# Performance work log

Measured on AMD Instinct MI355X. Metric: run time of the kernel, lower is better.

Reference implementation:

```python
import jax, jax.numpy as jnp
import numpy as np

B, H, W, C = 2, 128, 128, 96
L = H * W
NUM_HEADS = 6
D_STATE = 16
DT_RANK = 6  # ceil(96/16)
D_CONV = 4
MLP_HIDDEN = 4 * C


def _layernorm(x, g, b, eps=1e-5):
    m = x.mean(-1, keepdims=True)
    v = x.var(-1, keepdims=True)
    return (x - m) * jax.lax.rsqrt(v + eps) * g + b


def _dwconv2d(x, w, b):
    # x: [B,C,H,W], w: [C,1,3,3] depthwise, padding=1 (torch 'same' for k=3)
    y = jax.lax.conv_general_dilated(x, w, (1, 1), [(1, 1), (1, 1)],
                                     dimension_numbers=('NCHW', 'OIHW', 'NCHW'),
                                     feature_group_count=x.shape[1])
    return y + b[None, :, None, None]


def _dwconv1d(x, w):
    # x: [B,C,L], w: [C,1,4]; torch padding='same' for even k=4 pads (1,2); bias is None (conv_bias//2 == 0)
    return jax.lax.conv_general_dilated(x, w, (1,), [(1, 2)],
                                        dimension_numbers=('NCH', 'OIH', 'NCH'),
                                        feature_group_count=x.shape[1])


def _rope(x):
    # x: [b, H, W, c]; 2D axial rotary embedding, k_max = c//4 per axis
    b, h, w, c = x.shape
    k_max = c // 4
    theta = 1.0 / (10000.0 ** (jnp.arange(k_max, dtype=jnp.float32) / k_max))
    ang_h = jnp.broadcast_to(jnp.arange(h, dtype=jnp.float32)[:, None, None] * theta, (h, w, k_max))
    ang_w = jnp.broadcast_to(jnp.arange(w, dtype=jnp.float32)[None, :, None] * theta, (h, w, k_max))
    angles = jnp.concatenate([ang_h, ang_w], -1)  # [h,w,c//2]
    cos, sin = jnp.cos(angles), jnp.sin(angles)
    xr, xi = x[..., 0::2], x[..., 1::2]  # consecutive pairs -> complex
    out_r = xr * cos - xi * sin
    out_i = xr * sin + xi * cos
    return jnp.stack([out_r, out_i], -1).reshape(x.shape)


def _linear_attention(x, qk_w, qk_b, lepe_w, lepe_b):
    # x: [b, n, c]
    b, n, c = x.shape
    hd = c // NUM_HEADS
    qk = x @ qk_w + qk_b  # [b,n,2c]
    q = jax.nn.elu(qk[..., :c]) + 1.0
    k = jax.nn.elu(qk[..., c:]) + 1.0
    v = x
    q_r = _rope(q.reshape(b, H, W, c)).reshape(b, n, NUM_HEADS, hd).transpose(0, 2, 1, 3)
    k_r = _rope(k.reshape(b, H, W, c)).reshape(b, n, NUM_HEADS, hd).transpose(0, 2, 1, 3)
    qh = q.reshape(b, n, NUM_HEADS, hd).transpose(0, 2, 1, 3)
    kh = k.reshape(b, n, NUM_HEADS, hd).transpose(0, 2, 1, 3)
    vh = v.reshape(b, n, NUM_HEADS, hd).transpose(0, 2, 1, 3)
    kmean = kh.mean(axis=2, keepdims=True)  # [b,h,1,hd]
    zden = 1.0 / (jnp.einsum('bhnd,bhmd->bhnm', qh, kmean) + 1e-6)  # [b,h,n,1]
    scale = n ** (-0.5)
    kv = jnp.einsum('bhnd,bhne->bhde', k_r * scale, vh * scale)  # [b,h,hd,hd]
    out = jnp.einsum('bhnd,bhde->bhne', q_r, kv) * zden
    out = out.transpose(0, 2, 1, 3).reshape(b, n, c)
    v2d = v.reshape(b, H, W, c).transpose(0, 3, 1, 2)
    lepe = _dwconv2d(v2d, lepe_w, lepe_b).transpose(0, 2, 3, 1).reshape(b, n, c)
    return out + lepe


def _selective_scan(u, delta, A, Bm, Cm, Dv):
    # u, delta: [b,d,l]; A: [d,n]; Bm, Cm: [b,n,l]; Dv: [d]
    dA = jnp.exp(jnp.einsum('bdl,dn->lbdn', delta, A))
    dBu = jnp.einsum('bdl,bnl,bdl->lbdn', delta, Bm, u)
    Ct = jnp.moveaxis(Cm, -1, 0)  # [l,b,n]

    def step(hcar, inp):
        dA_t, dBu_t, C_t = inp
        hcar = dA_t * hcar + dBu_t  # [b,d,n]
        y_t = jnp.einsum('bdn,bn->bd', hcar, C_t)
        return hcar, y_t

    h0 = jnp.zeros(dA.shape[1:], dtype=u.dtype)
    _, ys = jax.lax.scan(step, h0, (dA, dBu, Ct))  # ys: [l,b,d]
    y = jnp.moveaxis(ys, 0, -1)  # [b,d,l]
    return y + Dv[None, :, None] * u


def setup_inputs() -> dict:
    key = jax.random.key(0)
    ks = iter(jax.random.split(key, 40))

    def rn(shape, s=0.02):
        return jax.random.normal(next(ks), shape, jnp.float32) * s

    dt = jnp.exp(jax.random.uniform(next(ks), (C,), jnp.float32)
                 * (np.log(0.1) - np.log(0.001)) + np.log(0.001))
    dt_proj_b = dt + jnp.log(-jnp.expm1(-dt))
    return {
        'hidden_states': jax.random.normal(next(ks), (B, L, C), jnp.float32),
        'norm_in_g': jnp.ones((C,), jnp.float32),
        'norm_in_b': jnp.zeros((C,), jnp.float32),
        'in_proj_w': rn((C, 3 * C)),
        'dw_w': rn((C, 1, 3, 3)),
        'dw_b': rn((C,)),
        'qk_w': rn((C, 2 * C)),
        'qk_b': rn((2 * C,)),
        'lepe_w': rn((C, 1, 3, 3)),
        'lepe_b': rn((C,)),
        'conv_x_w': rn((C, 1, D_CONV)),
        'conv_z_w': rn((C, 1, D_CONV)),
        'x_proj_w': rn((C, DT_RANK + 2 * D_STATE)),
        'dt_proj_w': rn((DT_RANK, C), DT_RANK ** -0.5),
        'dt_proj_b': dt_proj_b,
        'A_log': jnp.log(jnp.broadcast_to(jnp.arange(1, D_STATE + 1, dtype=jnp.float32), (C, D_STATE)) + 0.0),
        'D': jnp.ones((C,), jnp.float32),
        'out_proj_w': rn((2 * C, C)),
        'proj_out_w': rn((C, C)),
        'proj_out_b': rn((C,)),
        'out_w': rn((2 * C, C)),
        'out_b': rn((C,)),
        'norm_mlp_g': jnp.ones((C,), jnp.float32),
        'norm_mlp_b': jnp.zeros((C,), jnp.float32),
        'fc1_w': rn((C, MLP_HIDDEN)),
        'fc1_b': rn((MLP_HIDDEN,)),
        'fc2_w': rn((MLP_HIDDEN, C)),
        'fc2_b': rn((C,)),
    }


def reference(hidden_states, norm_in_g, norm_in_b, in_proj_w, dw_w, dw_b, qk_w, qk_b,
              lepe_w, lepe_b, conv_x_w, conv_z_w, x_proj_w, dt_proj_w, dt_proj_b,
              A_log, D, out_proj_w, proj_out_w, proj_out_b, out_w, out_b,
              norm_mlp_g, norm_mlp_b, fc1_w, fc1_b, fc2_w, fc2_b):
    b, l, c = hidden_states.shape
    shortcut = hidden_states
    hs = _layernorm(hidden_states, norm_in_g, norm_in_b)
    xzw = jnp.transpose(hs @ in_proj_w, (0, 2, 1))  # [b,3c,l]
    x, z, w_ = jnp.split(xzw, 3, axis=1)  # each [b,c,l]
    # linear-attention branch
    lin_x = jax.nn.silu(_dwconv2d(w_.reshape(b, c, H, W), dw_w, dw_b))
    lin_x = jnp.transpose(lin_x, (0, 2, 3, 1)).reshape(b, l, c)
    lin_x = _linear_attention(lin_x, qk_w, qk_b, lepe_w, lepe_b)
    # selective-scan branch
    A = -jnp.exp(A_log)
    x = jax.nn.silu(_dwconv1d(x, conv_x_w))
    z = jax.nn.silu(_dwconv1d(z, conv_z_w))
    x_dbl = jnp.einsum('bdl,de->ble', x, x_proj_w)
    dt = x_dbl[..., :DT_RANK]
    Bm = jnp.transpose(x_dbl[..., DT_RANK:DT_RANK + D_STATE], (0, 2, 1))
    Cm = jnp.transpose(x_dbl[..., DT_RANK + D_STATE:], (0, 2, 1))
    delta = jax.nn.softplus(jnp.einsum('blr,rd->bdl', dt, dt_proj_w) + dt_proj_b[None, :, None])
    y = _selective_scan(x, delta, A, Bm, Cm, D)
    y = jnp.concatenate([y, z], axis=1)  # [b,2c,l]
    out1 = jnp.transpose(y, (0, 2, 1)) @ out_proj_w  # [b,l,c]
    z_t = jnp.transpose(z, (0, 2, 1))
    out2 = (lin_x * z_t) @ proj_out_w + proj_out_b
    out = jnp.concatenate([out1, out2], -1) @ out_w + out_b
    out = shortcut + out
    h2 = _layernorm(out, norm_mlp_g, norm_mlp_b)
    h2 = jax.nn.gelu(h2 @ fc1_w + fc1_b, approximate=False)
    return out + (h2 @ fc2_w + fc2_b)
```

## Files before the change

kernel.cpp:

```cpp
#include <hip/hip_runtime.h>
#include <hip/hip_bf16.h>
#include <math.h>

#define B_ 2
#define H_ 128
#define W_ 128
#define C_ 96
#define L_ (H_*W_)
#define BL_ (B_*L_)
#define NH_ 6
#define NPROJ_ 38
#define MLPH_ 384
#define NCH_ 512
#define CHL_ (L_/NCH_)
#define NG_ 32

typedef __attribute__((ext_vector_type(8))) short bf16x8;
typedef __attribute__((ext_vector_type(4))) float f32x4;

#define MFMA16(a,b,c) __builtin_amdgcn_mfma_f32_16x16x32_bf16(a,b,c,0,0,0)

#define WOFF1 0
#define WOFF2 54
#define WOFF3 90
#define WOFF4 126
#define WOFF5 144
#define WOFF6 180
#define WOFF7 252
#define WOFF8 324
#define WFRAGS 333

__device__ __forceinline__ float siluf(float x){ return x / (1.f + __expf(-x)); }
__device__ __forceinline__ unsigned short f2bf(float x){
    __hip_bfloat16 h = __float2bfloat16(x);
    return *reinterpret_cast<unsigned short*>(&h);
}
__device__ __forceinline__ unsigned pack2(float a, float b){
    return (unsigned)f2bf(a) | ((unsigned)f2bf(b) << 16);
}
__device__ __forceinline__ float bf2f(unsigned short u){
    return __uint_as_float((unsigned)u << 16);
}
__device__ __forceinline__ float gelu_fast(float x){
    float u_ = 0.7978845608f*x*(1.f + 0.044715f*x*x);
    float au = fabsf(u_);
    float e = __expf(-2.f*au);
    float th = (1.f - e)/(1.f + e);
    th = copysignf(th, u_);
    return 0.5f*x*(1.f + th);
}

__global__ __launch_bounds__(64) void k_setup(const float* __restrict__ w1,
    const float* __restrict__ w2, const float* __restrict__ w3,
    const float* __restrict__ w4, const float* __restrict__ w5,
    const float* __restrict__ w6, const float* __restrict__ w7,
    const float* __restrict__ dww, const float* __restrict__ lw,
    const float* __restrict__ xpw, const float* __restrict__ cxw,
    const float* __restrict__ czw,
    unsigned short* __restrict__ dst, float2* __restrict__ ctab,
    float* __restrict__ wt9, float* __restrict__ lw9, float* __restrict__ kvacc,
    float* __restrict__ wxT, float* __restrict__ wzT)
{
    int m = blockIdx.y;
    int l = threadIdx.x;
    if (m < 7){
        const float* srcs[7] = {w1,w2,w3,w4,w5,w6,w7};
        const int Ks[7]   = {96,96,192,96,192,96,384};
        const int Ns[7]   = {288,192,96,96,96,384,96};
        const int offs[7] = {WOFF1,WOFF2,WOFF3,WOFF4,WOFF5,WOFF6,WOFF7};
        int f = blockIdx.x;
        int nnt = Ns[m] >> 4, nkf = Ks[m] >> 5;
        if (f >= nnt*nkf) return;
        int kf = f / nnt, nt = f - kf*nnt;
        const float* s = srcs[m];
        unsigned short* d = dst + ((size_t)(offs[m] + f)*64 + l)*8;
        int krow = kf*32 + (l>>4)*8;
        int col  = nt*16 + (l&15);
        #pragma unroll
        for (int j=0;j<8;j++) d[j] = f2bf(s[(size_t)(krow+j)*Ns[m] + col]);
    } else {
        int x = blockIdx.x;
        if (x == 0){
            for (int i=l; i<128*24; i+=64){
                int pos = i/24, p = i%24;
                float th = powf(10000.f, -(float)p/24.f);
                float sn, cs; sincosf((float)pos*th, &sn, &cs);
                ctab[i] = make_float2(cs, sn);
            }
        } else if (x == 1){
            for (int i=l; i<3264; i+=64) kvacc[i] = 0.f;
        } else if (x == 2){
            for (int i=l; i<864; i+=64){
                int c = i/9, tap = i%9;
                wt9[tap*96 + c] = dww[i];
                lw9[tap*96 + c] = lw[i];
            }
        } else if (x == 3){
            for (int f=0; f<9; f++){
                int kf=f/3, nt=f%3;
                unsigned short* d = dst + ((size_t)(WOFF8 + f)*64 + l)*8;
                int krow = kf*32 + (l>>4)*8;
                int col  = nt*16 + (l&15);
                #pragma unroll
                for (int j=0;j<8;j++){
                    float v = (col < NPROJ_) ? xpw[(size_t)(krow+j)*NPROJ_ + col] : 0.f;
                    d[j] = f2bf(v);
                }
            }
        } else if (x == 4){
            for (int i=l; i<384; i+=64){
                int j = i/96, c = i%96;
                wxT[i] = cxw[c*4 + j];
                wzT[i] = czw[c*4 + j];
            }
        }
    }
}

__global__ __launch_bounds__(256) void k_ln_inproj_m(const float* __restrict__ hs,
    const float* __restrict__ gg, const float* __restrict__ bb,
    const unsigned short* __restrict__ wbf,
    float* __restrict__ xx, float* __restrict__ zz, float* __restrict__ ww)
{
    __shared__ unsigned short A[64*128];
    int t = threadIdx.x;
    size_t row0 = (size_t)blockIdx.x * 64;
    {
        int r = t >> 2, q = t & 3;
        const float* src = hs + (row0 + r)*C_ + q*24;
        float v[24];
        float s=0.f, s2=0.f;
        #pragma unroll
        for (int i=0;i<24;i++){ float x=src[i]; v[i]=x; s+=x; s2+=x*x; }
        s += __shfl_xor(s,1); s2 += __shfl_xor(s2,1);
        s += __shfl_xor(s,2); s2 += __shfl_xor(s2,2);
        float mn = s*(1.f/C_);
        float rs = rsqrtf(s2*(1.f/C_) - mn*mn + 1e-5f);
        int base = r*128, sw = (r&7)<<3;
        #pragma unroll
        for (int i=0;i<24;i+=2){
            int c = q*24 + i;
            float a0 = (v[i]  -mn)*rs*gg[c]   + bb[c];
            float a1 = (v[i+1]-mn)*rs*gg[c+1] + bb[c+1];
            *(unsigned*)&A[base + (c ^ sw)] = pack2(a0,a1);
        }
    }
    __syncthreads();
    int w = t>>6, l = t&63, lr = l&15, lh = l>>4;
    int arow = w*16 + lr;
    int abase = arow*128, asw = (arow&7)<<3;
    bf16x8 af[3];
    #pragma unroll
    for (int kf=0;kf<3;kf++)
        af[kf] = *(const bf16x8*)&A[abase + ((kf*32 + lh*8) ^ asw)];
    #pragma unroll 2
    for (int nt=0; nt<18; nt++){
        f32x4 acc = {0.f,0.f,0.f,0.f};
        #pragma unroll
        for (int kf=0;kf<3;kf++){
            bf16x8 bf_ = *(const bf16x8*)(wbf + ((size_t)((WOFF1 + kf*18 + nt)*64 + l))*8);
            acc = MFMA16(af[kf], bf_, acc);
        }
        float* base_;
        if (nt < 6) base_ = xx; else if (nt < 12) base_ = zz; else base_ = ww;
        int col = (nt%6)*16 + lr;
        float* dst = base_ + (row0 + w*16 + lh*4)*C_ + col;
        #pragma unroll
        for (int j=0;j<4;j++) dst[(size_t)j*C_] = acc[j];
    }
}

__global__ __launch_bounds__(256) void k_dwconv2d(const float* __restrict__ wwb,
    const float* __restrict__ wt9, const float* __restrict__ dwb,
    float* __restrict__ out)
{
    int gid = blockIdx.x*256 + threadIdx.x;
    int row = gid/24, c4 = gid%24; int c = c4*4;
    int b = row >> 14;
    int ll = row & (L_-1);
    int h = ll >> 7, wq = ll & 127;
    float4 acc = {0.f,0.f,0.f,0.f};
    #pragma unroll
    for (int kh=0; kh<3; kh++){
        int hh = h + kh - 1;
        if ((unsigned)hh < 128u){
            int base_row = (b<<14) + (hh<<7);
            #pragma unroll
            for (int kw=0; kw<3; kw++){
                int wp = wq + kw - 1;
                if ((unsigned)wp < 128u){
                    float4 v = *(const float4*)&wwb[(size_t)(base_row + wp)*C_ + c];
                    float4 wt = *(const float4*)&wt9[(kh*3+kw)*96 + c];
                    acc.x += v.x*wt.x; acc.y += v.y*wt.y;
                    acc.z += v.z*wt.z; acc.w += v.w*wt.w;
                }
            }
        }
    }
    float4 bv = *(const float4*)&dwb[c];
    float4 o;
    o.x = siluf(acc.x+bv.x); o.y = siluf(acc.y+bv.y);
    o.z = siluf(acc.z+bv.z); o.w = siluf(acc.w+bv.w);
    *(float4*)&out[(size_t)row*C_ + c] = o;
}

__global__ __launch_bounds__(256) void k_conv1d_xdbl(const float* __restrict__ xxb,
    const float* __restrict__ zzb, const float* __restrict__ wxT,
    const float* __restrict__ wzT, const unsigned short* __restrict__ wbf,
    const float* __restrict__ dtw, const float* __restrict__ dtb,
    float* __restrict__ xs, float* __restrict__ zs,
    float* __restrict__ delta, float* __restrict__ BC)
{
    __shared__ unsigned short A[64*128];
    __shared__ float XD[64][8];
    __shared__ float dtws[6][96];
    int t = threadIdx.x;
    size_t row0 = (size_t)blockIdx.x * 64;
    int b = (int)(row0 >> 14);
    int l0 = (int)(row0 & 16383);
    for (int i=t; i<576; i+=256) dtws[i/96][i%96] = dtw[i];
    for (int p=t; p<64*24; p+=256){
        int r = p/24, cq = p - r*24, c = cq*4;
        int l = l0 + r;
        float ax0=0.f,ax1=0.f,ax2=0.f,ax3=0.f;
        float az0=0.f,az1=0.f,az2=0.f,az3=0.f;
        #pragma unroll
        for (int j=0;j<4;j++){
            int lq = l - 1 + j;
            if ((unsigned)lq < (unsigned)L_){
                size_t off = ((size_t)(b<<14) + lq)*C_ + c;
                float4 xv = *(const float4*)&xxb[off];
                float4 zv = *(const float4*)&zzb[off];
                float4 wx4 = *(const float4*)&wxT[j*96 + c];
                float4 wz4 = *(const float4*)&wzT[j*96 + c];
                ax0 += xv.x*wx4.x; ax1 += xv.y*wx4.y; ax2 += xv.z*wx4.z; ax3 += xv.w*wx4.w;
                az0 += zv.x*wz4.x; az1 += zv.y*wz4.y; az2 += zv.z*wz4.z; az3 += zv.w*wz4.w;
            }
        }
        ax0=siluf(ax0); ax1=siluf(ax1); ax2=siluf(ax2); ax3=siluf(ax3);
        az0=siluf(az0); az1=siluf(az1); az2=siluf(az2); az3=siluf(az3);
        float4 xo={ax0,ax1,ax2,ax3}, zo={az0,az1,az2,az3};
        *(float4*)&xs[(row0+r)*C_ + c] = xo;
        *(float4*)&zs[(row0+r)*C_ + c] = zo;
        int sw = (r&7)<<3;
        uint2 pk = { pack2(ax0,ax1), pack2(ax2,ax3) };
        *(uint2*)&A[r*128 + (c ^ sw)] = pk;
    }
    __syncthreads();
    int w=t>>6, l=t&63, lr=l&15, lh=l>>4;
    int arow = w*16+lr, asw=(arow&7)<<3;
    bf16x8 af[3];
    #pragma unroll
    for (int kf=0;kf<3;kf++)
        af[kf] = *(const bf16x8*)&A[arow*128 + ((kf*32 + lh*8) ^ asw)];
    #pragma unroll
    for (int nt=0; nt<3; nt++){
        f32x4 acc={0.f,0.f,0.f,0.f};
        #pragma unroll
        for (int kf=0;kf<3;kf++){
            bf16x8 bfr=*(const bf16x8*)(wbf + ((size_t)((WOFF8 + kf*3 + nt)*64 + l))*8);
            acc = MFMA16(af[kf], bfr, acc);
        }
        int col = nt*16 + lr;
        #pragma unroll
        for (int j=0;j<4;j++){
            int row = w*16 + lh*4 + j;
            if (col < 6) XD[row][col] = acc[j];
            else if (col < NPROJ_) BC[(row0+row)*32 + (col-6)] = acc[j];
        }
    }
    __syncthreads();
    {
        int r = t>>2, q = t&3;
        float xd0=XD[r][0], xd1=XD[r][1], xd2=XD[r][2];
        float xd3=XD[r][3], xd4=XD[r][4], xd5=XD[r][5];
        #pragma unroll
        for (int g=0; g<6; g++){
            int c = q*24 + g*4;
            float4 acc = *(const float4*)&dtb[c];
            float4 w0 = *(const float4*)&dtws[0][c];
            float4 w1 = *(const float4*)&dtws[1][c];
            float4 w2 = *(const float4*)&dtws[2][c];
            float4 w3 = *(const float4*)&dtws[3][c];
            float4 w4 = *(const float4*)&dtws[4][c];
            float4 w5 = *(const float4*)&dtws[5][c];
            acc.x += xd0*w0.x + xd1*w1.x + xd2*w2.x + xd3*w3.x + xd4*w4.x + xd5*w5.x;
            acc.y += xd0*w0.y + xd1*w1.y + xd2*w2.y + xd3*w3.y + xd4*w4.y + xd5*w5.y;
            acc.z += xd0*w0.z + xd1*w1.z + xd2*w2.z + xd3*w3.z + xd4*w4.z + xd5*w5.z;
            acc.w += xd0*w0.w + xd1*w1.w + xd2*w2.w + xd3*w3.w + xd4*w4.w + xd5*w5.w;
            float4 dl;
            dl.x = (acc.x>20.f)? acc.x : __logf(1.f+__expf(acc.x));
            dl.y = (acc.y>20.f)? acc.y : __logf(1.f+__expf(acc.y));
            dl.z = (acc.z>20.f)? acc.z : __logf(1.f+__expf(acc.z));
            dl.w = (acc.w>20.f)? acc.w : __logf(1.f+__expf(acc.w));
            *(float4*)&delta[(row0+r)*C_ + c] = dl;
        }
    }
}

__global__ __launch_bounds__(256) void k_qk_kv(const float* __restrict__ lin,
    const unsigned short* __restrict__ wbf, const float* __restrict__ qkb,
    const float2* __restrict__ ctab, float* __restrict__ qo,
    float* __restrict__ kvacc)
{
    __shared__ unsigned short A[64*128];
    __shared__ float KR[64*105];
    __shared__ float kmsum[96];
    int t = threadIdx.x;
    size_t row0 = (size_t)blockIdx.x * 64;
    int b = (int)(row0 >> 14);
    int l0 = (int)(row0 & 16383);
    for (int p = t; p < 64*48; p += 256){
        int r = p/48, c = (p - r*48)*2;
        float2 xy = *(const float2*)&lin[(row0 + r)*C_ + c];
        *(unsigned*)&A[r*128 + (c ^ ((r&7)<<3))] = pack2(xy.x, xy.y);
    }
    if (t < 96) kmsum[t] = 0.f;
    __syncthreads();
    int w=t>>6, l=t&63, lr=l&15, lh=l>>4;
    int arow = w*16+lr; int asw=(arow&7)<<3;
    bf16x8 af[3];
    #pragma unroll
    for (int kf=0;kf<3;kf++)
        af[kf] = *(const bf16x8*)&A[arow*128 + ((kf*32 + lh*8) ^ asw)];
    #pragma unroll 2
    for (int nt=0; nt<12; nt++){
        f32x4 acc={0.f,0.f,0.f,0.f};
        #pragma unroll
        for (int kf=0;kf<3;kf++){
            bf16x8 bfr=*(const bf16x8*)(wbf + ((size_t)((WOFF2 + kf*12 + nt)*64 + l))*8);
            acc = MFMA16(af[kf], bfr, acc);
        }
        int colg = nt*16 + lr;
        float bias = qkb[colg];
        float vv[4];
        #pragma unroll
        for (int j=0;j<4;j++){
            float v = acc[j] + bias;
            vv[j] = (v>0.f)? v+1.f : __expf(v);
        }
        if (nt < 6){
            float* dp = qo + (row0 + w*16 + lh*4)*C_ + colg;
            #pragma unroll
            for (int j=0;j<4;j++) dp[(size_t)j*C_] = vv[j];
        } else {
            int ck = colg - 96;
            atomicAdd(&kmsum[ck], vv[0]+vv[1]+vv[2]+vv[3]);
            float pv[4];
            #pragma unroll
            for (int j=0;j<4;j++) pv[j] = __shfl_xor(vv[j], 1);
            int p = ck >> 1;
            #pragma unroll
            for (int j=0;j<4;j++){
                int rl = l0 + w*16 + lh*4 + j;
                int hp = rl>>7, wp = rl&127;
                float2 cssn = (p<24)? ctab[hp*24+p] : ctab[wp*24+(p-24)];
                float kr = (ck&1)? (pv[j]*cssn.y + vv[j]*cssn.x)
                                 : (vv[j]*cssn.x - pv[j]*cssn.y);
                KR[(w*16+lh*4+j)*105 + ck] = kr;
            }
        }
    }
    __syncthreads();
    if (w < 2){
        #pragma unroll
        for (int hh=0; hh<3; hh++){
            int h = w*3 + hh;
            f32x4 acc = {0.f,0.f,0.f,0.f};
            #pragma unroll
            for (int kk=0; kk<2; kk++){
                union { bf16x8 v; unsigned short u[8]; } afu, bfu;
                #pragma unroll
                for (int j=0;j<8;j++){
                    int rr = kk*32 + lh*8 + j;
                    afu.u[j] = f2bf(KR[rr*105 + h*16 + lr]);
                    bfu.u[j] = A[rr*128 + ((h*16+lr) ^ ((rr&7)<<3))];
                }
                acc = MFMA16(afu.v, bfu.v, acc);
            }
            #pragma unroll
            for (int i=0;i<4;i++)
                atomicAdd(&kvacc[b*1536 + h*256 + (lh*4+i)*16 + lr], acc[i]);
        }
    }
    if (t < 96) atomicAdd(&kvacc[3072 + b*96 + t], kmsum[t]);
}

__global__ __launch_bounds__(384) void k_attnout(const float* __restrict__ qbuf,
    const float* __restrict__ vbuf, const float* __restrict__ kvacc,
    const float2* __restrict__ ctab, const float* __restrict__ lw9,
    const float* __restrict__ lb, float* __restrict__ aout)
{
    __shared__ float kvs[1536];
    __shared__ float kms[96];
    int t = threadIdx.x;
    size_t row0 = (size_t)blockIdx.x * 16;
    int b = (int)(row0 >> 14);
    const float invL = 1.f/16384.f;
    for (int i=t; i<1536; i+=384) kvs[i] = kvacc[b*1536+i]*invL;
    if (t < 96) kms[t] = kvacc[3072+b*96+t]*invL;
    __syncthreads();
    int r = t/24, c4 = t%24;
    int c = c4*4;
    int lrow = (int)(row0 & 16383) + r;
    int hp = lrow>>7, wp = lrow&127;
    size_t row = row0 + r;
    float4 q4 = *(const float4*)&qbuf[row*C_ + c];
    int p0 = c>>1, p1 = p0+1;
    float2 cs0 = (p0<24)? ctab[hp*24+p0] : ctab[wp*24+(p0-24)];
    float2 cs1 = (p1<24)? ctab[hp*24+p1] : ctab[wp*24+(p1-24)];
    float4 qr;
    qr.x = q4.x*cs0.x - q4.y*cs0.y;
    qr.y = q4.x*cs0.y + q4.y*cs0.x;
    qr.z = q4.z*cs1.x - q4.w*cs1.y;
    qr.w = q4.z*cs1.y + q4.w*cs1.x;
    int h = c4>>2, j = c4&3;
    int dbase = j*4;
    float zp = q4.x*kms[h*16+dbase]   + q4.y*kms[h*16+dbase+1]
             + q4.z*kms[h*16+dbase+2] + q4.w*kms[h*16+dbase+3];
    zp += __shfl_xor(zp,1);
    zp += __shfl_xor(zp,2);
    float zd = 1.f/(zp + 1e-6f);
    float4 o = {0.f,0.f,0.f,0.f};
    #pragma unroll
    for (int g=0; g<4; g++){
        float4 qg;
        if (g==0) qg = qr;
        else {
            qg.x=__shfl_xor(qr.x,g); qg.y=__shfl_xor(qr.y,g);
            qg.z=__shfl_xor(qr.z,g); qg.w=__shfl_xor(qr.w,g);
        }
        int db = ((j^g)<<2);
        const float* kp = &kvs[h*256 + db*16 + j*4];
        #pragma unroll
        for (int i=0;i<4;i++){
            float qi = (i==0)?qg.x:(i==1)?qg.y:(i==2)?qg.z:qg.w;
            float4 kv4 = *(const float4*)&kp[i*16];
            o.x += qi*kv4.x; o.y += qi*kv4.y;
            o.z += qi*kv4.z; o.w += qi*kv4.w;
        }
    }
    float4 acc = *(const float4*)&lb[c];
    #pragma unroll
    for (int kh=0; kh<3; kh++){
        int hh = hp + kh - 1;
        if ((unsigned)hh < 128u){
            int base_row = (b<<14) + (hh<<7);
            #pragma unroll
            for (int kw=0; kw<3; kw++){
                int wq = wp + kw - 1;
                if ((unsigned)wq < 128u){
                    float4 v = *(const float4*)&vbuf[(size_t)(base_row + wq)*C_ + c];
                    float4 wt = *(const float4*)&lw9[(kh*3+kw)*96 + c];
                    acc.x += v.x*wt.x; acc.y += v.y*wt.y;
                    acc.z += v.z*wt.z; acc.w += v.w*wt.w;
                }
            }
        }
    }
    float4 res;
    res.x = o.x*zd + acc.x; res.y = o.y*zd + acc.y;
    res.z = o.z*zd + acc.z; res.w = o.w*zd + acc.w;
    *(float4*)&aout[row*C_ + c] = res;
}

__global__ __launch_bounds__(384) void k_scan1(const float* __restrict__ delta,
    const float* __restrict__ xs, const float* __restrict__ BC,
    const float* __restrict__ A_log, float* __restrict__ Ap, float* __restrict__ Be)
{
    int t = threadIdx.x; int nq = t&3, c = t>>2;
    int blk = blockIdx.x; int b = blk>>9, ch = blk&(NCH_-1);
    float4 a4 = *(const float4*)&A_log[c*16 + nq*4];
    float a0=-__expf(a4.x), a1=-__expf(a4.y), a2=-__expf(a4.z), a3=-__expf(a4.w);
    float ap0=1.f,ap1=1.f,ap2=1.f,ap3=1.f;
    float be0=0.f,be1=0.f,be2=0.f,be3=0.f;
    size_t base = ((size_t)b<<14) + ch*CHL_;
    for (int i=0;i<CHL_;i++){
        size_t row = base + i;
        float dl = delta[row*C_+c];
        float u  = xs[row*C_+c];
        float du = dl*u;
        float4 bc = *(const float4*)&BC[row*32 + nq*4];
        float e0=__expf(dl*a0), e1=__expf(dl*a1), e2=__expf(dl*a2), e3=__expf(dl*a3);
        ap0*=e0; be0=be0*e0+du*bc.x;
        ap1*=e1; be1=be1*e1+du*bc.y;
        ap2*=e2; be2=be2*e2+du*bc.z;
        ap3*=e3; be3=be3*e3+du*bc.w;
    }
    size_t o = (size_t)blk*1536 + c*16 + nq*4;
    float4 apv={ap0,ap1,ap2,ap3}, bev={be0,be1,be2,be3};
    *(float4*)&Ap[o] = apv;
    *(float4*)&Be[o] = bev;
}

__global__ __launch_bounds__(384) void k_scan2a(const float* __restrict__ Ap,
    const float* __restrict__ Be, float* __restrict__ GA, float* __restrict__ GB)
{
    int t = threadIdx.x; int blk = blockIdx.x;
    int b = blk>>5, g = blk&(NG_-1);
    int idx = (t>>2)*16 + (t&3)*4;
    float4 A = {1.f,1.f,1.f,1.f}, Bv = {0.f,0.f,0.f,0.f};
    for (int j=0;j<16;j++){
        size_t o = ((size_t)(b*NCH_ + g*16 + j))*1536 + idx;
        float4 a = *(const float4*)&Ap[o];
        float4 bb = *(const float4*)&Be[o];
        Bv.x=a.x*Bv.x+bb.x; Bv.y=a.y*Bv.y+bb.y; Bv.z=a.z*Bv.z+bb.z; Bv.w=a.w*Bv.w+bb.w;
        A.x*=a.x; A.y*=a.y; A.z*=a.z; A.w*=a.w;
    }
    size_t o = (size_t)blk*1536 + idx;
    *(float4*)&GA[o] = A;
    *(float4*)&GB[o] = Bv;
}

__global__ __launch_bounds__(256) void k_scan2b(const float* __restrict__ GA,
    const float* __restrict__ GB, float* __restrict__ Gin)
{
    int t = blockIdx.x*256 + threadIdx.x;
    int b = t/1536, m = t%1536;
    float h = 0.f;
    for (int g=0; g<NG_; g++){
        size_t o = ((size_t)(b*NG_+g))*1536 + m;
        Gin[o] = h;
        h = GA[o]*h + GB[o];
    }
}

__global__ __launch_bounds__(384) void k_scan2c(const float* __restrict__ Ap,
    const float* __restrict__ Be, const float* __restrict__ Gin,
    float* __restrict__ Hin)
{
    int t = threadIdx.x; int blk = blockIdx.x;
    int b = blk>>5, g = blk&(NG_-1);
    int idx = (t>>2)*16 + (t&3)*4;
    float4 h = *(const float4*)&Gin[(size_t)blk*1536 + idx];
    for (int j=0;j<16;j++){
        size_t o = ((size_t)(b*NCH_ + g*16 + j))*1536 + idx;
        *(float4*)&Hin[o] = h;
        float4 a = *(const float4*)&Ap[o];
        float4 bb = *(const float4*)&Be[o];
        h.x=a.x*h.x+bb.x; h.y=a.y*h.y+bb.y; h.z=a.z*h.z+bb.z; h.w=a.w*h.w+bb.w;
    }
}

__global__ __launch_bounds__(384) void k_scan3(const float* __restrict__ delta,
    const float* __restrict__ xs, const float* __restrict__ BC,
    const float* __restrict__ A_log, const float* __restrict__ Dv,
    const float* __restrict__ Hin, float* __restrict__ y)
{
    int t = threadIdx.x; int nq = t&3, c = t>>2;
    int blk = blockIdx.x; int b = blk>>9, ch = blk&(NCH_-1);
    float4 a4 = *(const float4*)&A_log[c*16 + nq*4];
    float a0=-__expf(a4.x), a1=-__expf(a4.y), a2=-__expf(a4.z), a3=-__expf(a4.w);
    float4 h = *(const float4*)&Hin[(size_t)blk*1536 + c*16 + nq*4];
    float Dc = Dv[c];
    size_t base = ((size_t)b<<14) + ch*CHL_;
    for (int i=0;i<CHL_;i++){
        size_t row = base + i;
        float dl = delta[row*C_+c];
        float u  = xs[row*C_+c];
        float du = dl*u;
        float4 bcB = *(const float4*)&BC[row*32 + nq*4];
        float4 bcC = *(const float4*)&BC[row*32 + 16 + nq*4];
        float e0=__expf(dl*a0), e1=__expf(dl*a1), e2=__expf(dl*a2), e3=__expf(dl*a3);
        h.x=h.x*e0+du*bcB.x; h.y=h.y*e1+du*bcB.y;
        h.z=h.z*e2+du*bcB.z; h.w=h.w*e3+du*bcB.w;
        float yv = h.x*bcC.x + h.y*bcC.y + h.z*bcC.z + h.w*bcC.w;
        yv += __shfl_xor(yv,1);
        yv += __shfl_xor(yv,2);
        if (nq == 0) y[row*C_+c] = yv + Dc*u;
    }
}

__global__ __launch_bounds__(256) void k_combine_mlp(const float* __restrict__ y,
    const float* __restrict__ zs, const float* __restrict__ aout,
    const unsigned short* __restrict__ wbf, const float* __restrict__ pob,
    const float* __restrict__ outb, const float* __restrict__ hs,
    const float* __restrict__ gg, const float* __restrict__ bb,
    const float* __restrict__ f1b, const float* __restrict__ f2b,
    float* __restrict__ outr)
{
    __shared__ __attribute__((aligned(16))) char POOL[65536];
    unsigned short* Y  = (unsigned short*)POOL;
    unsigned short* AZ = (unsigned short*)(POOL + 24576);
    unsigned short* C2 = (unsigned short*)(POOL + 40960);
    unsigned short* AT = (unsigned short*)POOL;
    unsigned short* HID= (unsigned short*)(POOL + 16384);
    int t=threadIdx.x;
    size_t row0=(size_t)blockIdx.x*64;
    for (int p=t;p<64*48;p+=256){
        int r=p/48, c=(p-r*48)*2;
        size_t g=(row0+r)*C_+c;
        float2 yv=*(const float2*)&y[g];
        float2 zv=*(const float2*)&zs[g];
        float2 av=*(const float2*)&aout[g];
        int sw=(r&7)<<3;
        *(unsigned*)&Y[r*192 + (c^sw)] = pack2(yv.x,yv.y);
        *(unsigned*)&Y[r*192 + ((96+c)^sw)] = pack2(zv.x,zv.y);
        *(unsigned*)&AZ[r*128 + (c^sw)] = pack2(av.x*zv.x, av.y*zv.y);
    }
    __syncthreads();
    int w=t>>6,l=t&63,lr=l&15,lh=l>>4;
    int arow=w*16+lr; int asw=(arow&7)<<3;
    bf16x8 af1[6], af2[3];
    #pragma unroll
    for (int kf=0;kf<6;kf++) af1[kf]=*(const bf16x8*)&Y[arow*192 + ((kf*32+lh*8)^asw)];
    #pragma unroll
    for (int kf=0;kf<3;kf++) af2[kf]=*(const bf16x8*)&AZ[arow*128 + ((kf*32+lh*8)^asw)];
    #pragma unroll 2
    for (int nt=0;nt<6;nt++){
        f32x4 a1={0.f,0.f,0.f,0.f}, a2={0.f,0.f,0.f,0.f};
        #pragma unroll
        for (int kf=0;kf<6;kf++){
            bf16x8 b=*(const bf16x8*)(wbf+((size_t)((WOFF3+kf*6+nt)*64+l))*8);
            a1=MFMA16(af1[kf],b,a1);
        }
        #pragma unroll
        for (int kf=0;kf<3;kf++){
            bf16x8 b=*(const bf16x8*)(wbf+((size_t)((WOFF4+kf*6+nt)*64+l))*8);
            a2=MFMA16(af2[kf],b,a2);
        }
        int col=nt*16+lr;
        float pb=pob[col];
        #pragma unroll
        for (int j=0;j<4;j++){
            int row=w*16+lh*4+j;
            int sw2=(row&7)<<3;
            C2[row*192 + (col^sw2)] = f2bf(a1[j]);
            C2[row*192 + ((96+col)^sw2)] = f2bf(a2[j]+pb);
        }
    }
    __syncthreads();
    bf16x8 af3[6];
    #pragma unroll
    for (int kf=0;kf<6;kf++) af3[kf]=*(const bf16x8*)&C2[arow*192 + ((kf*32+lh*8)^asw)];
    float outv[6][4];
    #pragma unroll 2
    for (int nt=0;nt<6;nt++){
        f32x4 acc={0.f,0.f,0.f,0.f};
        #pragma unroll
        for (int kf=0;kf<6;kf++){
            bf16x8 b=*(const bf16x8*)(wbf+((size_t)((WOFF5+kf*6+nt)*64+l))*8);
            acc=MFMA16(af3[kf],b,acc);
        }
        int col=nt*16+lr;
        float ob=outb[col];
        #pragma unroll
        for (int j=0;j<4;j++){
            size_t row=row0+w*16+lh*4+j;
            outv[nt][j] = acc[j] + ob + hs[row*C_+col];
        }
    }
    float s_[4], s2_[4];
    #pragma unroll
    for (int j=0;j<4;j++){
        float s=0.f, s2=0.f;
        #pragma unroll
        for (int nt=0;nt<6;nt++){ float v=outv[nt][j]; s+=v; s2+=v*v; }
        s_[j]=s; s2_[j]=s2;
    }
    #pragma unroll
    for (int m=1;m<16;m<<=1){
        #pragma unroll
        for (int j=0;j<4;j++){
            s_[j]  += __shfl_xor(s_[j],  m);
            s2_[j] += __shfl_xor(s2_[j], m);
        }
    }
    __syncthreads();
    #pragma unroll
    for (int j=0;j<4;j++){
        float mn = s_[j]*(1.f/C_);
        float rs = rsqrtf(s2_[j]*(1.f/C_) - mn*mn + 1e-5f);
        int row = w*16+lh*4+j;
        int sw2 = (row&7)<<3;
        #pragma unroll
        for (int nt=0;nt<6;nt++){
            int col = nt*16+lr;
            AT[row*128 + (col^sw2)] = f2bf((outv[nt][j]-mn)*rs*gg[col]+bb[col]);
        }
    }
    __syncthreads();
    {
        bf16x8 af[3];
        #pragma unroll
        for(int kf=0;kf<3;kf++) af[kf]=*(const bf16x8*)&AT[arow*128+((kf*32+lh*8)^asw)];
        #pragma unroll 2
        for(int nt=0;nt<24;nt++){
            f32x4 acc={0.f,0.f,0.f,0.f};
            #pragma unroll
            for(int kf=0;kf<3;kf++){
                bf16x8 b=*(const bf16x8*)(wbf+((size_t)((WOFF6+kf*24+nt)*64+l))*8);
                acc=MFMA16(af[kf],b,acc);
            }
            int col=nt*16+lr;
            float bias=f1b[col];
            #pragma unroll
            for(int j=0;j<4;j++){
                int row=w*16+lh*4+j;
                HID[row*384 + (col^((row&7)<<3))] = f2bf(gelu_fast(acc[j]+bias));
            }
        }
    }
    __syncthreads();
    {
        bf16x8 afh[12];
        #pragma unroll
        for(int kf=0;kf<12;kf++) afh[kf]=*(const bf16x8*)&HID[arow*384+((kf*32+lh*8)^asw)];
        #pragma unroll 2
        for(int nt=0;nt<6;nt++){
            f32x4 acc={0.f,0.f,0.f,0.f};
            #pragma unroll
            for(int kf=0;kf<12;kf++){
                bf16x8 b=*(const bf16x8*)(wbf+((size_t)((WOFF7+kf*6+nt)*64+l))*8);
                acc=MFMA16(afh[kf],b,acc);
            }
            int col=nt*16+lr;
            float bias=f2b[col];
            #pragma unroll
            for(int j=0;j<4;j++){
                size_t row=row0+w*16+lh*4+j;
                outr[row*C_+col] = outv[nt][j] + acc[j] + bias;
            }
        }
    }
}

extern "C" void kernel_launch(void* const* d_in, const int* in_sizes, int n_in,
                              void* d_out, int out_size, void* d_ws, size_t ws_size,
                              hipStream_t stream)
{
    const float* hs        = (const float*)d_in[0];
    const float* norm_in_g = (const float*)d_in[1];
    const float* norm_in_b = (const float*)d_in[2];
    const float* in_proj_w = (const float*)d_in[3];
    const float* dw_w      = (const float*)d_in[4];
    const float* dw_b      = (const float*)d_in[5];
    const float* qk_w      = (const float*)d_in[6];
    const float* qk_b      = (const float*)d_in[7];
    const float* lepe_w    = (const float*)d_in[8];
    const float* lepe_b    = (const float*)d_in[9];
    const float* conv_x_w  = (const float*)d_in[10];
    const float* conv_z_w  = (const float*)d_in[11];
    const float* x_proj_w  = (const float*)d_in[12];
    const float* dt_proj_w = (const float*)d_in[13];
    const float* dt_proj_b = (const float*)d_in[14];
    const float* A_log     = (const float*)d_in[15];
    const float* Dv        = (const float*)d_in[16];
    const float* out_proj_w= (const float*)d_in[17];
    const float* proj_out_w= (const float*)d_in[18];
    const float* proj_out_b= (const float*)d_in[19];
    const float* out_w     = (const float*)d_in[20];
    const float* out_b     = (const float*)d_in[21];
    const float* norm_mlp_g= (const float*)d_in[22];
    const float* norm_mlp_b= (const float*)d_in[23];
    const float* fc1_w     = (const float*)d_in[24];
    const float* fc1_b     = (const float*)d_in[25];
    const float* fc2_w     = (const float*)d_in[26];
    const float* fc2_b     = (const float*)d_in[27];

    float* ws = (float*)d_ws;
    size_t o = 0;
    float* xx    = ws + o; o += (size_t)BL_*C_;
    float* zz    = ws + o; o += (size_t)BL_*C_;
    float* wwb   = ws + o; o += (size_t)BL_*C_;
    float* lin_x = ws + o; o += (size_t)BL_*C_;
    float* xs    = ws + o; o += (size_t)BL_*C_;
    float* zs    = ws + o; o += (size_t)BL_*C_;
    float* delta = ws + o; o += (size_t)BL_*C_;
    float* BC    = ws + o; o += (size_t)BL_*32;
    float* Ap    = ws + o; o += (size_t)B_*NCH_*1536;
    float* Be    = ws + o; o += (size_t)B_*NCH_*1536;
    float* Hin   = ws + o; o += (size_t)B_*NCH_*1536;
    float* GA    = ws + o; o += (size_t)B_*NG_*1536;
    float* GB    = ws + o; o += (size_t)B_*NG_*1536;
    float* Gin   = ws + o; o += (size_t)B_*NG_*1536;
    float* kvacc = ws + o; o += 3264;
    float2* ctab = (float2*)(ws + o); o += 6144;
    float* wt9   = ws + o; o += 864;
    float* lw9   = ws + o; o += 864;
    float* wxT   = ws + o; o += 384;
    float* wzT   = ws + o; o += 384;
    unsigned short* wbf = (unsigned short*)(ws + o);

    float* qbuf = xx;
    float* ybuf = zz;
    float* aout = wwb;
    float* outr = (float*)d_out;

    k_setup<<<dim3(72,8), 64, 0, stream>>>(in_proj_w, qk_w, out_proj_w, proj_out_w,
                                           out_w, fc1_w, fc2_w, dw_w, lepe_w,
                                           x_proj_w, conv_x_w, conv_z_w,
                                           wbf, ctab, wt9, lw9, kvacc, wxT, wzT);
    k_ln_inproj_m<<<BL_/64, 256, 0, stream>>>(hs, norm_in_g, norm_in_b, wbf, xx, zz, wwb);
    k_dwconv2d<<<(BL_*24)/256, 256, 0, stream>>>(wwb, wt9, dw_b, lin_x);
    k_conv1d_xdbl<<<BL_/64, 256, 0, stream>>>(xx, zz, wxT, wzT, wbf,
                                              dt_proj_w, dt_proj_b, xs, zs, delta, BC);
    k_qk_kv<<<BL_/64, 256, 0, stream>>>(lin_x, wbf, qk_b, ctab, qbuf, kvacc);
    k_attnout<<<BL_/16, 384, 0, stream>>>(qbuf, lin_x, kvacc, ctab, lw9, lepe_b, aout);
    k_scan1<<<B_*NCH_, 384, 0, stream>>>(delta, xs, BC, A_log, Ap, Be);
    k_scan2a<<<B_*NG_, 384, 0, stream>>>(Ap, Be, GA, GB);
    k_scan2b<<<12, 256, 0, stream>>>(GA, GB, Gin);
    k_scan2c<<<B_*NG_, 384, 0, stream>>>(Ap, Be, Gin, Hin);
    k_scan3<<<B_*NCH_, 384, 0, stream>>>(delta, xs, BC, A_log, Dv, Hin, ybuf);
    k_combine_mlp<<<BL_/64, 256, 0, stream>>>(ybuf, zs, aout, wbf, proj_out_b,
                                              out_b, hs, norm_mlp_g, norm_mlp_b,
                                              fc1_b, fc2_b, outr);
}
```

Measured before the change: 209.1 us.

## Split combine_mlp output columns across two waves per row tile; spread kv MFMA

k_combine_mlp now launches 512 threads, with two waves per 16-row tile that each compute half of the output columns for every GEMM stage. LayerNorm partial sums are exchanged through a small shared array. The aim is more waves per block and less serial MFMA work per wave. The kv accumulation in k_qk_kv now spreads the six heads over all four waves instead of two. The cost is more register pressure per block, an extra shared-memory reduction step, and duplicated A-fragment loads.

```diff
diff --git a/kernel.cpp b/kernel.cpp
--- a/kernel.cpp
+++ b/kernel.cpp
@@ -362,26 +362,22 @@
         }
     }
     __syncthreads();
-    if (w < 2){
-        #pragma unroll
-        for (int hh=0; hh<3; hh++){
-            int h = w*3 + hh;
-            f32x4 acc = {0.f,0.f,0.f,0.f};
-            #pragma unroll
-            for (int kk=0; kk<2; kk++){
-                union { bf16x8 v; unsigned short u[8]; } afu, bfu;
-                #pragma unroll
-                for (int j=0;j<8;j++){
-                    int rr = kk*32 + lh*8 + j;
-                    afu.u[j] = f2bf(KR[rr*105 + h*16 + lr]);
-                    bfu.u[j] = A[rr*128 + ((h*16+lr) ^ ((rr&7)<<3))];
-                }
-                acc = MFMA16(afu.v, bfu.v, acc);
-            }
-            #pragma unroll
-            for (int i=0;i<4;i++)
-                atomicAdd(&kvacc[b*1536 + h*256 + (lh*4+i)*16 + lr], acc[i]);
-        }
+    for (int h = w; h < 6; h += 4){
+        f32x4 acc = {0.f,0.f,0.f,0.f};
+        #pragma unroll
+        for (int kk=0; kk<2; kk++){
+            union { bf16x8 v; unsigned short u[8]; } afu, bfu;
+            #pragma unroll
+            for (int j=0;j<8;j++){
+                int rr = kk*32 + lh*8 + j;
+                afu.u[j] = f2bf(KR[rr*105 + h*16 + lr]);
+                bfu.u[j] = A[rr*128 + ((h*16+lr) ^ ((rr&7)<<3))];
+            }
+            acc = MFMA16(afu.v, bfu.v, acc);
+        }
+        #pragma unroll
+        for (int i=0;i<4;i++)
+            atomicAdd(&kvacc[b*1536 + h*256 + (lh*4+i)*16 + lr], acc[i]);
     }
     if (t < 96) atomicAdd(&kvacc[3072 + b*96 + t], kmsum[t]);
 }
@@ -571,7 +567,7 @@
     }
 }
 
-__global__ __launch_bounds__(256) void k_combine_mlp(const float* __restrict__ y,
+__global__ __launch_bounds__(512) void k_combine_mlp(const float* __restrict__ y,
     const float* __restrict__ zs, const float* __restrict__ aout,
     const unsigned short* __restrict__ wbf, const float* __restrict__ pob,
     const float* __restrict__ outb, const float* __restrict__ hs,
@@ -580,6 +576,7 @@
     float* __restrict__ outr)
 {
     __shared__ __attribute__((aligned(16))) char POOL[65536];
+    __shared__ float LNS[64][2], LNS2[64][2];
     unsigned short* Y  = (unsigned short*)POOL;
     unsigned short* AZ = (unsigned short*)(POOL + 24576);
     unsigned short* C2 = (unsigned short*)(POOL + 40960);
@@ -587,7 +584,7 @@
     unsigned short* HID= (unsigned short*)(POOL + 16384);
     int t=threadIdx.x;
     size_t row0=(size_t)blockIdx.x*64;
-    for (int p=t;p<64*48;p+=256){
+    for (int p=t;p<64*48;p+=512){
         int r=p/48, c=(p-r*48)*2;
         size_t g=(row0+r)*C_+c;
         float2 yv=*(const float2*)&y[g];
@@ -599,15 +596,17 @@
         *(unsigned*)&AZ[r*128 + (c^sw)] = pack2(av.x*zv.x, av.y*zv.y);
     }
     __syncthreads();
-    int w=t>>6,l=t&63,lr=l&15,lh=l>>4;
-    int arow=w*16+lr; int asw=(arow&7)<<3;
+    int w=t>>6, l=t&63, lr=l&15, lh=l>>4;
+    int rt=w>>1, hf=w&1;
+    int arow=rt*16+lr; int asw=(arow&7)<<3;
     bf16x8 af1[6], af2[3];
     #pragma unroll
     for (int kf=0;kf<6;kf++) af1[kf]=*(const bf16x8*)&Y[arow*192 + ((kf*32+lh*8)^asw)];
     #pragma unroll
     for (int kf=0;kf<3;kf++) af2[kf]=*(const bf16x8*)&AZ[arow*128 + ((kf*32+lh*8)^asw)];
-    #pragma unroll 2
-    for (int nt=0;nt<6;nt++){
+    #pragma unroll
+    for (int q=0;q<3;q++){
+        int nt = hf*3 + q;
         f32x4 a1={0.f,0.f,0.f,0.f}, a2={0.f,0.f,0.f,0.f};
         #pragma unroll
         for (int kf=0;kf<6;kf++){
@@ -623,7 +622,7 @@
         float pb=pob[col];
         #pragma unroll
         for (int j=0;j<4;j++){
-            int row=w*16+lh*4+j;
+            int row=rt*16+lh*4+j;
             int sw2=(row&7)<<3;
             C2[row*192 + (col^sw2)] = f2bf(a1[j]);
             C2[row*192 + ((96+col)^sw2)] = f2bf(a2[j]+pb);
@@ -633,9 +632,10 @@
     bf16x8 af3[6];
     #pragma unroll
     for (int kf=0;kf<6;kf++) af3[kf]=*(const bf16x8*)&C2[arow*192 + ((kf*32+lh*8)^asw)];
-    float outv[6][4];
-    #pragma unroll 2
-    for (int nt=0;nt<6;nt++){
+    float outv[3][4];
+    #pragma unroll
+    for (int q=0;q<3;q++){
+        int nt = hf*3 + q;
         f32x4 acc={0.f,0.f,0.f,0.f};
         #pragma unroll
         for (int kf=0;kf<6;kf++){
@@ -646,8 +646,8 @@
         float ob=outb[col];
         #pragma unroll
         for (int j=0;j<4;j++){
-            size_t row=row0+w*16+lh*4+j;
-            outv[nt][j] = acc[j] + ob + hs[row*C_+col];
+            size_t row=row0+rt*16+lh*4+j;
+            outv[q][j] = acc[j] + ob + hs[row*C_+col];
         }
     }
     float s_[4], s2_[4];
@@ -655,7 +655,7 @@
     for (int j=0;j<4;j++){
         float s=0.f, s2=0.f;
         #pragma unroll
-        for (int nt=0;nt<6;nt++){ float v=outv[nt][j]; s+=v; s2+=v*v; }
+        for (int q=0;q<3;q++){ float v=outv[q][j]; s+=v; s2+=v*v; }
         s_[j]=s; s2_[j]=s2;
     }
     #pragma unroll
@@ -666,17 +666,27 @@
             s2_[j] += __shfl_xor(s2_[j], m);
         }
     }
+    if (lr==0){
+        #pragma unroll
+        for (int j=0;j<4;j++){
+            int row = rt*16+lh*4+j;
+            LNS[row][hf]  = s_[j];
+            LNS2[row][hf] = s2_[j];
+        }
+    }
     __syncthreads();
     #pragma unroll
     for (int j=0;j<4;j++){
-        float mn = s_[j]*(1.f/C_);
-        float rs = rsqrtf(s2_[j]*(1.f/C_) - mn*mn + 1e-5f);
-        int row = w*16+lh*4+j;
+        int row = rt*16+lh*4+j;
+        float s  = LNS[row][0]  + LNS[row][1];
+        float s2 = LNS2[row][0] + LNS2[row][1];
+        float mn = s*(1.f/C_);
+        float rs = rsqrtf(s2*(1.f/C_) - mn*mn + 1e-5f);
         int sw2 = (row&7)<<3;
         #pragma unroll
-        for (int nt=0;nt<6;nt++){
-            int col = nt*16+lr;
-            AT[row*128 + (col^sw2)] = f2bf((outv[nt][j]-mn)*rs*gg[col]+bb[col]);
+        for (int q=0;q<3;q++){
+            int col = (hf*3+q)*16+lr;
+            AT[row*128 + (col^sw2)] = f2bf((outv[q][j]-mn)*rs*gg[col]+bb[col]);
         }
     }
     __syncthreads();
@@ -685,7 +695,8 @@
         #pragma unroll
         for(int kf=0;kf<3;kf++) af[kf]=*(const bf16x8*)&AT[arow*128+((kf*32+lh*8)^asw)];
         #pragma unroll 2
-        for(int nt=0;nt<24;nt++){
+        for(int q=0;q<12;q++){
+            int nt = hf*12 + q;
             f32x4 acc={0.f,0.f,0.f,0.f};
             #pragma unroll
             for(int kf=0;kf<3;kf++){
@@ -696,7 +707,7 @@
             float bias=f1b[col];
             #pragma unroll
             for(int j=0;j<4;j++){
-                int row=w*16+lh*4+j;
+                int row=rt*16+lh*4+j;
                 HID[row*384 + (col^((row&7)<<3))] = f2bf(gelu_fast(acc[j]+bias));
             }
         }
@@ -706,8 +717,9 @@
         bf16x8 afh[12];
         #pragma unroll
         for(int kf=0;kf<12;kf++) afh[kf]=*(const bf16x8*)&HID[arow*384+((kf*32+lh*8)^asw)];
-        #pragma unroll 2
-        for(int nt=0;nt<6;nt++){
+        #pragma unroll
+        for(int q=0;q<3;q++){
+            int nt = hf*3 + q;
             f32x4 acc={0.f,0.f,0.f,0.f};
             #pragma unroll
             for(int kf=0;kf<12;kf++){
@@ -718,8 +730,8 @@
             float bias=f2b[col];
             #pragma unroll
             for(int j=0;j<4;j++){
-                size_t row=row0+w*16+lh*4+j;
-                outr[row*C_+col] = outv[nt][j] + acc[j] + bias;
+                size_t row=row0+rt*16+lh*4+j;
+                outr[row*C_+col] = outv[q][j] + acc[j] + bias;
             }
         }
     }
@@ -802,7 +814,7 @@
     k_scan2b<<<12, 256, 0, stream>>>(GA, GB, Gin);
     k_scan2c<<<B_*NG_, 384, 0, stream>>>(Ap, Be, Gin, Hin);
     k_scan3<<<B_*NCH_, 384, 0, stream>>>(delta, xs, BC, A_log, Dv, Hin, ybuf);
-    k_combine_mlp<<<BL_/64, 256, 0, stream>>>(ybuf, zs, aout, wbf, proj_out_b,
+    k_combine_mlp<<<BL_/64, 512, 0, stream>>>(ybuf, zs, aout, wbf, proj_out_b,
                                               out_b, hs, norm_mlp_g, norm_mlp_b,
                                               fc1_b, fc2_b, outr);
 }
```

Result: faster. 203.2 us (-2.8%).
